# Kernel optimization log

Hardware: AMD Instinct MI355X
Metric: run time of the kernel (lower is better)

Reference implementation:

```python
import jax, jax.numpy as jnp
import numpy as np

B, S, H = 2, 2048, 1024
N_HEAD = 16
HEAD_DIM = H // N_HEAD


def setup_inputs() -> dict:
    key = jax.random.key(0)
    ks = jax.random.split(key, 8)
    init = 0.02
    return {
        "hidden_states": jax.random.normal(ks[0], (B, S, H), dtype=jnp.float32),
        "residual": jax.random.normal(ks[1], (B, S, H), dtype=jnp.float32),
        "alibi": jax.random.normal(ks[2], (B * N_HEAD, 1, S), dtype=jnp.float32),
        "attention_mask": jnp.ones((B, S), dtype=bool),
        "w_qkv": jax.random.normal(ks[3], (H, 3 * H), dtype=jnp.float32) * init,
        "b_qkv": jax.random.normal(ks[4], (3 * H,), dtype=jnp.float32) * init,
        "w_o": jax.random.normal(ks[5], (H, H), dtype=jnp.float32) * init,
        "b_o": jax.random.normal(ks[6], (H,), dtype=jnp.float32) * init,
        "layer_number": 4,
    }


def reference(hidden_states, residual, alibi, attention_mask, w_qkv, b_qkv, w_o, b_o, layer_number):
    b, s, h = hidden_states.shape
    nh, hd = N_HEAD, HEAD_DIM
    # fused QKV projection: (B,S,3H) -> (B,S,nh,3*hd) -> split
    fused_qkv = (hidden_states @ w_qkv + b_qkv).reshape(b, s, nh, 3 * hd)
    query, key, value = jnp.split(fused_qkv, 3, axis=-1)  # each (B,S,nh,hd)

    L = max(int(layer_number), 1)
    alpha = 1.0 / (np.sqrt(hd).astype(np.float32) * L)
    beta = 1.0 / L

    # scores = beta*alibi + alpha * q@k^T, reshaped to (B,nh,Sq,Sk)
    scores = jnp.einsum("bqnh,bknh->bnqk", query, key) * alpha
    scores = scores + beta * alibi.reshape(b, nh, 1, s)
    # FlaxBloomScaledSoftmax applies scale = layer_number before masking
    scores = scores * L

    # fused causal + padding mask (attention_mask_func): keep = causal & pad_q & pad_k
    causal = jnp.tril(jnp.ones((s, s), dtype=bool))
    pad = attention_mask  # (B,S) bool, True = attend
    keep = causal[None, None, :, :] & pad[:, None, :, None] & pad[:, None, None, :]  # (B,1,S,S)

    masked_scores = jnp.where(keep, scores, jnp.float32(-10000.0))
    probs = jax.nn.softmax(masked_scores.astype(jnp.float32), axis=-1) * keep
    probs = probs.astype(hidden_states.dtype)

    context = jnp.einsum("bnqk,bknh->bqnh", probs, value).reshape(b, s, h)
    attn_output = context @ w_o + b_o + residual
    return attn_output
```

## Files before the change

kernel.cpp:

```cpp
#include <hip/hip_runtime.h>
#include <hip/hip_bf16.h>

#define S_LEN 2048
#define HID   1024
#define NHEAD 16
#define HDIM  64
#define NBH   32

#define QSCALE 0.18033688f
#define LOG2E  1.44269504f

typedef __attribute__((ext_vector_type(8))) short short8;
typedef __attribute__((ext_vector_type(4))) float f32x4;

__device__ inline void gload_lds16(const void* g, void* l) {
  __builtin_amdgcn_global_load_lds(
      (const __attribute__((address_space(1))) void*)g,
      (__attribute__((address_space(3))) void*)l, 16, 0, 0);
}

__device__ inline ushort f2bf(float f) {
  __hip_bfloat16 h = __float2bfloat16(f);
  return *reinterpret_cast<const ushort*>(&h);
}

__device__ inline float exp2_fast(float x) {
  float r;
  asm("v_exp_f32 %0, %1" : "=v"(r) : "v"(x));
  return r;
}

__global__ __launch_bounds__(256) void convert_bf16(
    const float* __restrict__ in, ushort* __restrict__ out, int n8)
{
    int i = blockIdx.x * 256 + threadIdx.x;
    if (i < n8) {
        float4 a = ((const float4*)in)[i * 2];
        float4 b = ((const float4*)in)[i * 2 + 1];
        union { ushort u[8]; uint4 v; } o;
        o.u[0]=f2bf(a.x); o.u[1]=f2bf(a.y); o.u[2]=f2bf(a.z); o.u[3]=f2bf(a.w);
        o.u[4]=f2bf(b.x); o.u[5]=f2bf(b.y); o.u[6]=f2bf(b.z); o.u[7]=f2bf(b.w);
        ((uint4*)out)[i] = o.v;
    }
}

__global__ __launch_bounds__(256) void transpose_convert(
    const float* __restrict__ in, ushort* __restrict__ out, int R, int C)
{
    __shared__ ushort Ls[64][72];
    const int c0 = blockIdx.x * 64, r0 = blockIdx.y * 64;
    const int t = threadIdx.x;
    const int tr = t >> 4, tc = (t & 15) * 4;
    #pragma unroll
    for (int i = 0; i < 4; ++i) {
        int gr = r0 + tr + i * 16;
        float4 v = *(const float4*)(in + (size_t)gr * C + c0 + tc);
        Ls[tc + 0][tr + i * 16] = f2bf(v.x);
        Ls[tc + 1][tr + i * 16] = f2bf(v.y);
        Ls[tc + 2][tr + i * 16] = f2bf(v.z);
        Ls[tc + 3][tr + i * 16] = f2bf(v.w);
    }
    __syncthreads();
    #pragma unroll
    for (int i = 0; i < 4; ++i) {
        int oc = c0 + tr + i * 16;
        ushort4 v = *(const ushort4*)&Ls[tr + i * 16][tc];
        *(ushort4*)(out + (size_t)oc * R + r0 + tc) = v;
    }
}

__global__ __launch_bounds__(512, 2) void qkv_gemm_mfma(
    const ushort* __restrict__ A, const ushort* __restrict__ Bt,
    const float* __restrict__ bias,
    ushort* __restrict__ Q, ushort* __restrict__ K, ushort* __restrict__ V)
{
    __shared__ __align__(16) ushort As[2][256 * 64];
    __shared__ __align__(16) ushort Bs[2][256 * 64];
    const int tid = threadIdx.x;
    const int l   = tid & 63;
    const int w   = tid >> 6;
    const int wm  = w >> 2;
    const int wn  = w & 3;
    const int l7  = l & 7, l15 = l & 15, g = l >> 4;
    const int srow = l >> 3;
    const int schunk = l7 ^ srow;

    int lin = blockIdx.y * 12 + blockIdx.x;
    int swz = (lin & 7) * 24 + (lin >> 3);
    const int m0 = (swz / 12) * 256;
    const int n0 = (swz % 12) * 256;

    f32x4 acc[8][4];
    #pragma unroll
    for (int i = 0; i < 8; ++i)
        #pragma unroll
        for (int j = 0; j < 4; ++j) acc[i][j] = (f32x4){0.f, 0.f, 0.f, 0.f};

#define STG_A(tt, qq) gload_lds16(A + (size_t)(m0 + (qq)*64 + w*8 + srow)*1024 \
                                    + (tt)*64 + schunk*8,                      \
                                  As[(tt) & 1] + ((qq)*64 + w*8)*64)
#define STG_B(tt, qq) gload_lds16(Bt + (size_t)(n0 + (qq)*64 + w*8 + srow)*1024 \
                                    + (tt)*64 + schunk*8,                       \
                                  Bs[(tt) & 1] + ((qq)*64 + w*8)*64)
#define LD_A(bb, mf, kk) (*(const short8*)(As[bb] + ((mf)*32 + wm*16 + l15)*64 \
                                           + ((((kk)*4 + g) ^ l7) << 3)))
#define LD_B(bb, nf, kk) (*(const short8*)(Bs[bb] + (wn*64 + (nf)*16 + l15)*64 \
                                           + ((((kk)*4 + g) ^ l7) << 3)))

    #pragma unroll
    for (int qq = 0; qq < 4; ++qq) { STG_A(0, qq); STG_B(0, qq); }
    #pragma unroll
    for (int qq = 0; qq < 3; ++qq) { STG_A(1, qq); STG_B(1, qq); }
    asm volatile("s_waitcnt vmcnt(6)" ::: "memory");
    __builtin_amdgcn_s_barrier();

    short8 bfr[8];

    for (int it = 0; it < 8; ++it) {
        const int t = 2 * it;
        #pragma unroll
        for (int ph = 0; ph < 4; ++ph) {
            short8 afr[4];
            afr[0] = LD_A(0, 2*ph,     0);
            afr[1] = LD_A(0, 2*ph,     1);
            afr[2] = LD_A(0, 2*ph + 1, 0);
            afr[3] = LD_A(0, 2*ph + 1, 1);
            if (ph == 0) {
                #pragma unroll
                for (int nf = 0; nf < 4; ++nf) {
                    bfr[nf*2 + 0] = LD_B(0, nf, 0);
                    bfr[nf*2 + 1] = LD_B(0, nf, 1);
                }
            }
            if (ph == 0) { STG_A(t + 1, 3); STG_B(t + 1, 3); }
            else if (t + 2 < 16) { STG_A(t + 2, ph - 1); STG_B(t + 2, ph - 1); }
            __builtin_amdgcn_s_barrier();
            asm volatile("s_waitcnt lgkmcnt(0)" ::: "memory");
            __builtin_amdgcn_sched_barrier(0);
            __builtin_amdgcn_s_setprio(1);
            #pragma unroll
            for (int kk = 0; kk < 2; ++kk)
                #pragma unroll
                for (int mi = 0; mi < 2; ++mi)
                    #pragma unroll
                    for (int nf = 0; nf < 4; ++nf)
                        acc[2*ph + mi][nf] = __builtin_amdgcn_mfma_f32_16x16x32_bf16(
                            afr[mi*2 + kk], bfr[nf*2 + kk], acc[2*ph + mi][nf], 0, 0, 0);
            __builtin_amdgcn_s_setprio(0);
            if (ph == 3) asm volatile("s_waitcnt vmcnt(6)" ::: "memory");
            __builtin_amdgcn_s_barrier();
        }
        #pragma unroll
        for (int ph = 0; ph < 4; ++ph) {
            short8 afr[4];
            afr[0] = LD_A(1, 2*ph,     0);
            afr[1] = LD_A(1, 2*ph,     1);
            afr[2] = LD_A(1, 2*ph + 1, 0);
            afr[3] = LD_A(1, 2*ph + 1, 1);
            if (ph == 0) {
                #pragma unroll
                for (int nf = 0; nf < 4; ++nf) {
                    bfr[nf*2 + 0] = LD_B(1, nf, 0);
                    bfr[nf*2 + 1] = LD_B(1, nf, 1);
                }
            }
            if (ph == 0) { if (t + 2 < 16) { STG_A(t + 2, 3); STG_B(t + 2, 3); } }
            else if (t + 3 < 16) { STG_A(t + 3, ph - 1); STG_B(t + 3, ph - 1); }
            __builtin_amdgcn_s_barrier();
            asm volatile("s_waitcnt lgkmcnt(0)" ::: "memory");
            __builtin_amdgcn_sched_barrier(0);
            __builtin_amdgcn_s_setprio(1);
            #pragma unroll
            for (int kk = 0; kk < 2; ++kk)
                #pragma unroll
                for (int mi = 0; mi < 2; ++mi)
                    #pragma unroll
                    for (int nf = 0; nf < 4; ++nf)
                        acc[2*ph + mi][nf] = __builtin_amdgcn_mfma_f32_16x16x32_bf16(
                            afr[mi*2 + kk], bfr[nf*2 + kk], acc[2*ph + mi][nf], 0, 0, 0);
            __builtin_amdgcn_s_setprio(0);
            if (ph == 3) asm volatile("s_waitcnt vmcnt(6)" ::: "memory");
            __builtin_amdgcn_s_barrier();
        }
    }
#undef STG_A
#undef STG_B
#undef LD_A
#undef LD_B

    #pragma unroll
    for (int nf = 0; nf < 4; ++nf) {
        int gcol = n0 + wn * 64 + nf * 16 + l15;
        int head = gcol / 192;
        int rem  = gcol - head * 192;
        int which = rem >> 6;
        int d     = rem & 63;
        float bv = bias[gcol];
        #pragma unroll
        for (int mf = 0; mf < 8; ++mf) {
            int grow = m0 + mf * 32 + wm * 16 + g * 4;
            int bb = grow >> 11;
            int ss = grow & 2047;
            int bhh = (bb << 4) + head;
            if (which == 2) {
                ushort4 pk;
                pk.x = f2bf(acc[mf][nf][0] + bv);
                pk.y = f2bf(acc[mf][nf][1] + bv);
                pk.z = f2bf(acc[mf][nf][2] + bv);
                pk.w = f2bf(acc[mf][nf][3] + bv);
                *(ushort4*)(V + ((size_t)bhh * 64 + d) * S_LEN + ss) = pk;
            } else {
                ushort* plane = (which == 0) ? Q : K;
                float sc = (which == 0) ? QSCALE : 1.0f;
                ushort* dst = plane + (((size_t)bhh * S_LEN + ss) << 6) + d;
                #pragma unroll
                for (int r = 0; r < 4; ++r)
                    dst[(size_t)r << 6] = f2bf((acc[mf][nf][r] + bv) * sc);
            }
        }
    }
}

#define GEMM_STAGE(A_, Bt_, kk0, buf) do {                                    \
    _Pragma("unroll")                                                         \
    for (int i = 0; i < 4; ++i) {                                             \
        int row = i * 32 + w * 8 + srow;                                      \
        gload_lds16(A_ + (size_t)(m0 + row) * 1024 + (kk0) + schunk * 8,      \
                    Asl[buf] + (i * 32 + w * 8) * 64);                        \
        gload_lds16(Bt_ + (size_t)(n0 + row) * 1024 + (kk0) + schunk * 8,     \
                    Bsl[buf] + (i * 32 + w * 8) * 64);                        \
    }                                                                         \
} while (0)

#define GEMM_CORE(A_, Bt_)                                                    \
    __shared__ ushort Asl[2][128 * 64];                                       \
    __shared__ ushort Bsl[2][128 * 64];                                       \
    const int tid = threadIdx.x;                                              \
    const int l = tid & 63;                                                   \
    const int w = tid >> 6;                                                   \
    const int wm = (w >> 1) * 64;                                             \
    const int wn = (w & 1) * 64;                                              \
    const int m0 = blockIdx.y * 128;                                          \
    const int n0 = blockIdx.x * 128;                                          \
    const int l15 = l & 15, g = l >> 4;                                       \
    const int srow = l >> 3;                                                  \
    const int schunk = (l & 7) ^ srow;                                        \
    f32x4 acc[4][4];                                                          \
    _Pragma("unroll")                                                         \
    for (int i = 0; i < 4; ++i)                                               \
        _Pragma("unroll")                                                     \
        for (int j = 0; j < 4; ++j) acc[i][j] = (f32x4){0.f, 0.f, 0.f, 0.f};  \
    GEMM_STAGE(A_, Bt_, 0, 0);                                                \
    __syncthreads();                                                          \
    for (int ks = 0; ks < 16; ++ks) {                                         \
        const int cur = ks & 1;                                               \
        if (ks < 15) GEMM_STAGE(A_, Bt_, (ks + 1) * 64, cur ^ 1);             \
        const ushort* Acur = Asl[cur];                                        \
        const ushort* Bcur = Bsl[cur];                                        \
        _Pragma("unroll")                                                     \
        for (int kk = 0; kk < 2; ++kk) {                                      \
            short8 af[4], bf[4];                                              \
            _Pragma("unroll")                                                 \
            for (int mf = 0; mf < 4; ++mf) {                                  \
                int row = wm + mf * 16 + l15;                                 \
                int ch = (kk * 4 + g) ^ (row & 7);                            \
                af[mf] = *(const short8*)(Acur + row * 64 + ch * 8);          \
            }                                                                 \
            _Pragma("unroll")                                                 \
            for (int nf = 0; nf < 4; ++nf) {                                  \
                int row = wn + nf * 16 + l15;                                 \
                int ch = (kk * 4 + g) ^ (row & 7);                            \
                bf[nf] = *(const short8*)(Bcur + row * 64 + ch * 8);          \
            }                                                                 \
            _Pragma("unroll")                                                 \
            for (int mf = 0; mf < 4; ++mf)                                    \
                _Pragma("unroll")                                             \
                for (int nf = 0; nf < 4; ++nf)                                \
                    acc[mf][nf] = __builtin_amdgcn_mfma_f32_16x16x32_bf16(    \
                        af[mf], bf[nf], acc[mf][nf], 0, 0, 0);                \
        }                                                                     \
        __syncthreads();                                                      \
    }

__global__ __launch_bounds__(256) void out_gemm_mfma(
    const ushort* __restrict__ A, const ushort* __restrict__ Bt,
    const float* __restrict__ bias, const float* __restrict__ resid,
    float* __restrict__ out)
{
    GEMM_CORE(A, Bt)
    #pragma unroll
    for (int nf = 0; nf < 4; ++nf) {
        int gcol = n0 + wn + nf * 16 + l15;
        float bv = bias[gcol];
        #pragma unroll
        for (int mf = 0; mf < 4; ++mf) {
            int grow = m0 + wm + mf * 16 + g * 4;
            #pragma unroll
            for (int r = 0; r < 4; ++r) {
                size_t idx = (size_t)(grow + r) * 1024 + gcol;
                out[idx] = acc[mf][nf][r] + bv + resid[idx];
            }
        }
    }
}

#define STAGE(tt, idx) do {                                                   \
    gload_lds16(Kbh + (size_t)((tt) * 64 + w * 8 + srow) * 64 + schunk * 8,   \
                Ks[idx] + (w * 8) * 64);                                      \
    gload_lds16(Vbh + (size_t)(w * 8 + srow) * S_LEN + (tt) * 64 + schunk * 8,\
                Vs[idx] + (w * 8) * 64);                                      \
} while (0)

#define QK_TILE(SN, tt, idx, FULL) do {                                       \
    const ushort* Kc = Ks[idx];                                               \
    _Pragma("unroll")                                                         \
    for (int kb = 0; kb < 4; ++kb) {                                          \
        float4 a4 = *(const float4*)&alib[(tt) * 64 + kb * 16 + g * 4];       \
        SN[kb] = (f32x4){a4.x, a4.y, a4.z, a4.w};                             \
        if (FULL || (tt) * 64 + kb * 16 <= qmax) {                            \
            int row = kb * 16 + l15;                                          \
            short8 ka0 = *(const short8*)(Kc + row * 64 + ((g ^ l7) << 3));   \
            short8 ka1 = *(const short8*)(Kc + row * 64 + (((4+g) ^ l7) << 3));\
            SN[kb] = __builtin_amdgcn_mfma_f32_16x16x32_bf16(ka0, qb0, SN[kb], 0, 0, 0); \
            SN[kb] = __builtin_amdgcn_mfma_f32_16x16x32_bf16(ka1, qb1, SN[kb], 0, 0, 0); \
        }                                                                     \
    }                                                                         \
} while (0)

#define SM_PV(SC, tt, idx, FULL) do {                                         \
    const ushort* Vc = Vs[idx];                                               \
    ushort* Pw = Ps[w];                                                       \
    float p[16];                                                              \
    _Pragma("unroll")                                                         \
    for (int kb = 0; kb < 4; ++kb) {                                          \
        _Pragma("unroll")                                                     \
        for (int r = 0; r < 4; ++r) {                                         \
            float s = SC[kb][r];                                              \
            if (!FULL) {                                                      \
                int kglob = (tt) * 64 + kb * 16 + g * 4 + r;                  \
                s = (kglob > qglob) ? -1e30f : s;                             \
            }                                                                 \
            p[kb * 4 + r] = s;                                                \
        }                                                                     \
    }                                                                         \
    float mx0 = fmaxf(fmaxf(p[0], p[1]),   fmaxf(p[2], p[3]));                \
    float mx1 = fmaxf(fmaxf(p[4], p[5]),   fmaxf(p[6], p[7]));                \
    float mx2 = fmaxf(fmaxf(p[8], p[9]),   fmaxf(p[10], p[11]));              \
    float mx3 = fmaxf(fmaxf(p[12], p[13]), fmaxf(p[14], p[15]));              \
    float pmax = fmaxf(fmaxf(mx0, mx1), fmaxf(mx2, mx3));                     \
    pmax = fmaxf(pmax, __shfl_xor(pmax, 16));                                 \
    pmax = fmaxf(pmax, __shfl_xor(pmax, 32));                                 \
    if (!__all(pmax <= m + 11.5415603f)) {          \
        float mn = fmaxf(m, pmax);                                            \
        float resc = exp2_fast(m - mn);                                       \
        m = mn; lsum *= resc;                                                 \
        _Pragma("unroll")                                                     \
        for (int nb = 0; nb < 4; ++nb) oacc[nb] *= resc;                      \
    }                                                                         \
    _Pragma("unroll")                                                         \
    for (int i = 0; i < 16; ++i) p[i] = exp2_fast(p[i] - m);                  \
    float sm0 = (p[0] + p[1]) + (p[2] + p[3]);                                \
    float sm1 = (p[4] + p[5]) + (p[6] + p[7]);                                \
    float sm2 = (p[8] + p[9]) + (p[10] + p[11]);                              \
    float sm3 = (p[12] + p[13]) + (p[14] + p[15]);                            \
    float rsum = (sm0 + sm1) + (sm2 + sm3);                                   \
    rsum += __shfl_xor(rsum, 16);                                             \
    rsum += __shfl_xor(rsum, 32);                                             \
    lsum += rsum;                                                             \
    _Pragma("unroll")                                                         \
    for (int kb = 0; kb < 4; ++kb) {                                          \
        ushort4 pk;                                                           \
        pk.x = f2bf(p[kb * 4 + 0]); pk.y = f2bf(p[kb * 4 + 1]);               \
        pk.z = f2bf(p[kb * 4 + 2]); pk.w = f2bf(p[kb * 4 + 3]);               \
        int chunk = kb * 2 + (g >> 1);                                        \
        *(ushort4*)(Pw + l15 * 64 + ((chunk ^ l7) << 3) + ((g & 1) << 2)) = pk;\
    }                                                                         \
    short8 pb0 = *(const short8*)(Pw + l15 * 64 + ((g ^ l7) << 3));           \
    short8 pb1 = *(const short8*)(Pw + l15 * 64 + (((4 + g) ^ l7) << 3));     \
    _Pragma("unroll")                                                         \
    for (int nb = 0; nb < 4; ++nb) {                                          \
        int row = nb * 16 + l15;                                              \
        short8 va0 = *(const short8*)(Vc + row * 64 + ((g ^ l7) << 3));       \
        oacc[nb] = __builtin_amdgcn_mfma_f32_16x16x32_bf16(va0, pb0, oacc[nb], 0, 0, 0); \
    }                                                                         \
    if (FULL || (tt) * 64 + 32 <= qmax) {                                     \
        _Pragma("unroll")                                                     \
        for (int nb = 0; nb < 4; ++nb) {                                      \
            int row = nb * 16 + l15;                                          \
            short8 va1 = *(const short8*)(Vc + row * 64 + (((4 + g) ^ l7) << 3)); \
            oacc[nb] = __builtin_amdgcn_mfma_f32_16x16x32_bf16(va1, pb1, oacc[nb], 0, 0, 0); \
        }                                                                     \
    }                                                                         \
} while (0)

__global__ __launch_bounds__(512, 4) void attn_mfma(
    const ushort* __restrict__ Qp, const ushort* __restrict__ Kp,
    const ushort* __restrict__ Vtp, const float* __restrict__ alibi,
    ushort* __restrict__ ctx)
{
    __shared__ ushort Ks[3][64 * 64];
    __shared__ ushort Vs[3][64 * 64];
    __shared__ ushort Ps[8][16 * 64];
    __shared__ __align__(16) float alib[S_LEN];

    const int bh  = blockIdx.y;
    const int qt  = (blockIdx.y & 16) ? (int)blockIdx.x : 15 - (int)blockIdx.x;
    const int tid = threadIdx.x;
    const int w   = tid >> 6;
    const int l   = tid & 63;
    const int l7  = l & 7, l15 = l & 15, g = l >> 4;
    const int q0  = qt * 128;

    const ushort* Qbh = Qp  + (size_t)bh * S_LEN * HDIM;
    const ushort* Kbh = Kp  + (size_t)bh * S_LEN * HDIM;
    const ushort* Vbh = Vtp + (size_t)bh * HDIM * S_LEN;
    const float*  abh = alibi + (size_t)bh * S_LEN;

    const int qglob = q0 + w * 16 + l15;
    const int qmax  = q0 + w * 16 + 15;
    const int qmin  = q0 + w * 16;

    short8 qb0 = *(const short8*)(Qbh + (size_t)qglob * 64 + g * 8);
    short8 qb1 = *(const short8*)(Qbh + (size_t)qglob * 64 + 32 + g * 8);

    float m = -1e30f, lsum = 0.f;
    f32x4 oacc[4];
    #pragma unroll
    for (int nb = 0; nb < 4; ++nb) oacc[nb] = (f32x4){0.f, 0.f, 0.f, 0.f};

    const int srow   = l >> 3;
    const int schunk = (l & 7) ^ srow;

    {
        float4 a = *(const float4*)(abh + tid * 4);
        a.x *= LOG2E; a.y *= LOG2E; a.z *= LOG2E; a.w *= LOG2E;
        *(float4*)(alib + tid * 4) = a;
    }
    STAGE(0, 0);
    __syncthreads();
    STAGE(1, 1);

    f32x4 sa[4], sb[4];
    QK_TILE(sa, 0, 0, 0);

    const int nt = 2 * qt + 2;
    int ipv = 0, iqk = 1, ist = 2;
    for (int t = 0; t < nt; t += 2) {
        __syncthreads();
        if (t + 2 < nt) STAGE(t + 2, ist);
        if ((t + 1 < nt) && ((t + 1) * 64 + 63 <= qmin)) {
            QK_TILE(sb, t + 1, iqk, 1);
            SM_PV(sa, t, ipv, 1);
        } else {
            if ((t + 1 < nt) && ((t + 1) * 64 <= qmax)) QK_TILE(sb, t + 1, iqk, 0);
            if (t * 64 <= qmax) SM_PV(sa, t, ipv, 0);
        }
        { int tmp = ipv; ipv = iqk; iqk = ist; ist = tmp; }

        __syncthreads();
        if (t + 3 < nt) STAGE(t + 3, ist);
        if ((t + 2 < nt) && ((t + 2) * 64 + 63 <= qmin)) {
            QK_TILE(sa, t + 2, iqk, 1);
            SM_PV(sb, t + 1, ipv, 1);
        } else {
            if ((t + 2 < nt) && ((t + 2) * 64 <= qmax)) QK_TILE(sa, t + 2, iqk, 0);
            if ((t + 1) * 64 <= qmax) SM_PV(sb, t + 1, ipv, 0);
        }
        { int tmp = ipv; ipv = iqk; iqk = ist; ist = tmp; }
    }

    const int bb = bh >> 4, hh = bh & 15;
    float inv = 1.0f / lsum;
    ushort* crow = ctx + (size_t)(bb * S_LEN + qglob) * 1024 + hh * 64;
    #pragma unroll
    for (int nb = 0; nb < 4; ++nb) {
        ushort4 pk;
        pk.x = f2bf(oacc[nb][0] * inv);
        pk.y = f2bf(oacc[nb][1] * inv);
        pk.z = f2bf(oacc[nb][2] * inv);
        pk.w = f2bf(oacc[nb][3] * inv);
        *(ushort4*)(crow + nb * 16 + g * 4) = pk;
    }
}

extern "C" void kernel_launch(void* const* d_in, const int* in_sizes, int n_in,
                              void* d_out, int out_size, void* d_ws, size_t ws_size,
                              hipStream_t stream) {
    const float* X      = (const float*)d_in[0];
    const float* resid  = (const float*)d_in[1];
    const float* alibi  = (const float*)d_in[2];
    const float* w_qkv  = (const float*)d_in[4];
    const float* b_qkv  = (const float*)d_in[5];
    const float* w_o    = (const float*)d_in[6];
    const float* b_o    = (const float*)d_in[7];

    const size_t plane = (size_t)NBH * S_LEN * HDIM;
    ushort* Xb   = (ushort*)d_ws;
    ushort* Wqkt = Xb + (size_t)4096 * 1024;
    ushort* Wot  = Wqkt + (size_t)3072 * 1024;
    ushort* Qb   = Wot + (size_t)1024 * 1024;
    ushort* Kb   = Qb + plane;
    ushort* Vbt  = Qb + 2 * plane;
    ushort* ctx  = Qb + 3 * plane;
    float*  out  = (float*)d_out;

    convert_bf16<<<2048, 256, 0, stream>>>(X, Xb, 4096 * 1024 / 8);
    dim3 gt1(3072 / 64, 1024 / 64);
    transpose_convert<<<gt1, 256, 0, stream>>>(w_qkv, Wqkt, 1024, 3072);
    dim3 gt2(1024 / 64, 1024 / 64);
    transpose_convert<<<gt2, 256, 0, stream>>>(w_o, Wot, 1024, 1024);

    dim3 g1(3072 / 256, 4096 / 256);
    qkv_gemm_mfma<<<g1, 512, 0, stream>>>(Xb, Wqkt, b_qkv, Qb, Kb, Vbt);

    dim3 g2(S_LEN / 128, NBH);
    attn_mfma<<<g2, 512, 0, stream>>>(Qb, Kb, Vbt, alibi, ctx);

    dim3 g3(1024 / 128, 4096 / 128);
    out_gemm_mfma<<<g3, 256, 0, stream>>>(ctx, Wot, b_o, resid, out);
}
```

Measured before the change: 125.5 us.

## Shrink attention LDS footprint: double-buffered K/V, streamed prescaled alibi, higher occupancy

Alibi prescaling by log2e moves into the bf16 conversion kernel, which writes the prescaled values to workspace. The attention kernel drops the 8KB full-row alibi LDS buffer and instead streams 64-entry alibi tiles into a small triple buffer. K and V staging changes from a shared triple buffer to double buffers indexed by tile parity, and V loads are issued one step later than K. Launch bounds rise from 4 to 6 blocks per CU to exploit the smaller LDS footprint. This trades some prefetch depth and register budget for occupancy, and relies on barrier ordering to keep the new buffer reuse safe.

```diff
diff --git a/kernel.cpp b/kernel.cpp
--- a/kernel.cpp
+++ b/kernel.cpp
@@ -31,16 +31,24 @@
 }
 
 __global__ __launch_bounds__(256) void convert_bf16(
-    const float* __restrict__ in, ushort* __restrict__ out, int n8)
+    const float* __restrict__ in, ushort* __restrict__ out, int n8,
+    const float* __restrict__ alibi, float* __restrict__ alibis)
 {
-    int i = blockIdx.x * 256 + threadIdx.x;
-    if (i < n8) {
-        float4 a = ((const float4*)in)[i * 2];
-        float4 b = ((const float4*)in)[i * 2 + 1];
-        union { ushort u[8]; uint4 v; } o;
-        o.u[0]=f2bf(a.x); o.u[1]=f2bf(a.y); o.u[2]=f2bf(a.z); o.u[3]=f2bf(a.w);
-        o.u[4]=f2bf(b.x); o.u[5]=f2bf(b.y); o.u[6]=f2bf(b.z); o.u[7]=f2bf(b.w);
-        ((uint4*)out)[i] = o.v;
+    if (blockIdx.x < 2048) {
+        int i = blockIdx.x * 256 + threadIdx.x;
+        if (i < n8) {
+            float4 a = ((const float4*)in)[i * 2];
+            float4 b = ((const float4*)in)[i * 2 + 1];
+            union { ushort u[8]; uint4 v; } o;
+            o.u[0]=f2bf(a.x); o.u[1]=f2bf(a.y); o.u[2]=f2bf(a.z); o.u[3]=f2bf(a.w);
+            o.u[4]=f2bf(b.x); o.u[5]=f2bf(b.y); o.u[6]=f2bf(b.z); o.u[7]=f2bf(b.w);
+            ((uint4*)out)[i] = o.v;
+        }
+    } else {
+        int j = (blockIdx.x - 2048) * 256 + threadIdx.x;
+        float4 a = ((const float4*)alibi)[j];
+        a.x *= LOG2E; a.y *= LOG2E; a.z *= LOG2E; a.w *= LOG2E;
+        ((float4*)alibis)[j] = a;
     }
 }
 
@@ -304,18 +312,22 @@
     }
 }
 
-#define STAGE(tt, idx) do {                                                   \
+#define STAGE_K(tt)                                                           \
     gload_lds16(Kbh + (size_t)((tt) * 64 + w * 8 + srow) * 64 + schunk * 8,   \
-                Ks[idx] + (w * 8) * 64);                                      \
+                Ks[(tt) & 1] + (w * 8) * 64)
+#define STAGE_V(tt)                                                           \
     gload_lds16(Vbh + (size_t)(w * 8 + srow) * S_LEN + (tt) * 64 + schunk * 8,\
-                Vs[idx] + (w * 8) * 64);                                      \
+                Vs[(tt) & 1] + (w * 8) * 64)
+#define STAGE_AB(tt) do {                                                     \
+    if (tid < 16) gload_lds16(abh + (tt) * 64 + tid * 4, ab3[(tt) % 3]);      \
 } while (0)
 
-#define QK_TILE(SN, tt, idx, FULL) do {                                       \
-    const ushort* Kc = Ks[idx];                                               \
+#define QK_TILE(SN, tt, FULL) do {                                            \
+    const ushort* Kc  = Ks[(tt) & 1];                                         \
+    const float*  abt = ab3[(tt) % 3];                                        \
     _Pragma("unroll")                                                         \
     for (int kb = 0; kb < 4; ++kb) {                                          \
-        float4 a4 = *(const float4*)&alib[(tt) * 64 + kb * 16 + g * 4];       \
+        float4 a4 = *(const float4*)&abt[kb * 16 + g * 4];                    \
         SN[kb] = (f32x4){a4.x, a4.y, a4.z, a4.w};                             \
         if (FULL || (tt) * 64 + kb * 16 <= qmax) {                            \
             int row = kb * 16 + l15;                                          \
@@ -327,8 +339,8 @@
     }                                                                         \
 } while (0)
 
-#define SM_PV(SC, tt, idx, FULL) do {                                         \
-    const ushort* Vc = Vs[idx];                                               \
+#define SM_PV(SC, tt, FULL) do {                                              \
+    const ushort* Vc = Vs[(tt) & 1];                                          \
     ushort* Pw = Ps[w];                                                       \
     float p[16];                                                              \
     _Pragma("unroll")                                                         \
@@ -393,15 +405,15 @@
     }                                                                         \
 } while (0)
 
-__global__ __launch_bounds__(512, 4) void attn_mfma(
+__global__ __launch_bounds__(512, 6) void attn_mfma(
     const ushort* __restrict__ Qp, const ushort* __restrict__ Kp,
-    const ushort* __restrict__ Vtp, const float* __restrict__ alibi,
+    const ushort* __restrict__ Vtp, const float* __restrict__ alibis,
     ushort* __restrict__ ctx)
 {
-    __shared__ ushort Ks[3][64 * 64];
-    __shared__ ushort Vs[3][64 * 64];
+    __shared__ ushort Ks[2][64 * 64];
+    __shared__ ushort Vs[2][64 * 64];
     __shared__ ushort Ps[8][16 * 64];
-    __shared__ __align__(16) float alib[S_LEN];
+    __shared__ __align__(16) float ab3[3][64];
 
     const int bh  = blockIdx.y;
     const int qt  = (blockIdx.y & 16) ? (int)blockIdx.x : 15 - (int)blockIdx.x;
@@ -414,7 +426,7 @@
     const ushort* Qbh = Qp  + (size_t)bh * S_LEN * HDIM;
     const ushort* Kbh = Kp  + (size_t)bh * S_LEN * HDIM;
     const ushort* Vbh = Vtp + (size_t)bh * HDIM * S_LEN;
-    const float*  abh = alibi + (size_t)bh * S_LEN;
+    const float*  abh = alibis + (size_t)bh * S_LEN;
 
     const int qglob = q0 + w * 16 + l15;
     const int qmax  = q0 + w * 16 + 15;
@@ -431,42 +443,35 @@
     const int srow   = l >> 3;
     const int schunk = (l & 7) ^ srow;
 
-    {
-        float4 a = *(const float4*)(abh + tid * 4);
-        a.x *= LOG2E; a.y *= LOG2E; a.z *= LOG2E; a.w *= LOG2E;
-        *(float4*)(alib + tid * 4) = a;
-    }
-    STAGE(0, 0);
+    STAGE_K(0); STAGE_K(1); STAGE_V(0); STAGE_AB(0); STAGE_AB(1);
     __syncthreads();
-    STAGE(1, 1);
 
     f32x4 sa[4], sb[4];
-    QK_TILE(sa, 0, 0, 0);
+    QK_TILE(sa, 0, 0);
 
     const int nt = 2 * qt + 2;
-    int ipv = 0, iqk = 1, ist = 2;
     for (int t = 0; t < nt; t += 2) {
         __syncthreads();
-        if (t + 2 < nt) STAGE(t + 2, ist);
-        if ((t + 1 < nt) && ((t + 1) * 64 + 63 <= qmin)) {
-            QK_TILE(sb, t + 1, iqk, 1);
-            SM_PV(sa, t, ipv, 1);
+        if (t + 2 < nt) { STAGE_K(t + 2); STAGE_AB(t + 2); }
+        STAGE_V(t + 1);
+        if ((t + 1) * 64 + 63 <= qmin) {
+            QK_TILE(sb, t + 1, 1);
+            SM_PV(sa, t, 1);
         } else {
-            if ((t + 1 < nt) && ((t + 1) * 64 <= qmax)) QK_TILE(sb, t + 1, iqk, 0);
-            if (t * 64 <= qmax) SM_PV(sa, t, ipv, 0);
-        }
-        { int tmp = ipv; ipv = iqk; iqk = ist; ist = tmp; }
+            if ((t + 1) * 64 <= qmax) QK_TILE(sb, t + 1, 0);
+            if (t * 64 <= qmax) SM_PV(sa, t, 0);
+        }
 
         __syncthreads();
-        if (t + 3 < nt) STAGE(t + 3, ist);
+        if (t + 3 < nt) { STAGE_K(t + 3); STAGE_AB(t + 3); }
+        if (t + 2 < nt) STAGE_V(t + 2);
         if ((t + 2 < nt) && ((t + 2) * 64 + 63 <= qmin)) {
-            QK_TILE(sa, t + 2, iqk, 1);
-            SM_PV(sb, t + 1, ipv, 1);
+            QK_TILE(sa, t + 2, 1);
+            SM_PV(sb, t + 1, 1);
         } else {
-            if ((t + 2 < nt) && ((t + 2) * 64 <= qmax)) QK_TILE(sa, t + 2, iqk, 0);
-            if ((t + 1) * 64 <= qmax) SM_PV(sb, t + 1, ipv, 0);
-        }
-        { int tmp = ipv; ipv = iqk; iqk = ist; ist = tmp; }
+            if ((t + 2 < nt) && ((t + 2) * 64 <= qmax)) QK_TILE(sa, t + 2, 0);
+            if ((t + 1) * 64 <= qmax) SM_PV(sb, t + 1, 0);
+        }
     }
 
     const int bb = bh >> 4, hh = bh & 15;
@@ -502,9 +507,11 @@
     ushort* Kb   = Qb + plane;
     ushort* Vbt  = Qb + 2 * plane;
     ushort* ctx  = Qb + 3 * plane;
+    float*  alibis = (float*)(ctx + plane);
     float*  out  = (float*)d_out;
 
-    convert_bf16<<<2048, 256, 0, stream>>>(X, Xb, 4096 * 1024 / 8);
+    convert_bf16<<<2048 + 64, 256, 0, stream>>>(X, Xb, 4096 * 1024 / 8,
+                                                alibi, alibis);
     dim3 gt1(3072 / 64, 1024 / 64);
     transpose_convert<<<gt1, 256, 0, stream>>>(w_qkv, Wqkt, 1024, 3072);
     dim3 gt2(1024 / 64, 1024 / 64);
@@ -514,7 +521,7 @@
     qkv_gemm_mfma<<<g1, 512, 0, stream>>>(Xb, Wqkt, b_qkv, Qb, Kb, Vbt);
 
     dim3 g2(S_LEN / 128, NBH);
-    attn_mfma<<<g2, 512, 0, stream>>>(Qb, Kb, Vbt, alibi, ctx);
+    attn_mfma<<<g2, 512, 0, stream>>>(Qb, Kb, Vbt, alibis, ctx);
 
     dim3 g3(1024 / 128, 4096 / 128);
     out_gemm_mfma<<<g3, 256, 0, stream>>>(ctx, Wot, b_o, resid, out);
```

Result: slower. 274.2 us (+118.6%).
